# Performance work log

Hardware: AMD Instinct MI355X
Metric: run time of the kernel (lower is better)

## Reference

```python
import jax, jax.numpy as jnp
import numpy as np

N = 50000        # num nodes (num_paths)
E = 1_600_000    # num edges (avg degree 32)
W = 64           # window_size -> x feature dim
H = 128          # hidden_dimension
TEMP = 1.0       # temperature


def setup_inputs() -> dict:
    key = jax.random.key(0)
    k = jax.random.split(key, 6)
    x = jax.random.normal(k[0], (N, W), dtype=jnp.float32)
    y = jax.random.normal(k[1], (N,), dtype=jnp.float32)
    edge_index = jax.random.randint(k[2], (2, E), 0, N, dtype=jnp.int32)
    w1 = jax.random.normal(k[3], (2 * W, H), dtype=jnp.float32) / np.sqrt(2 * W)
    b1 = jnp.zeros((H,), dtype=jnp.float32)
    w2 = jax.random.normal(k[4], (H, 1), dtype=jnp.float32) / np.sqrt(H)
    b2 = jnp.zeros((1,), dtype=jnp.float32)
    return {"x": x, "y": y, "edge_index": edge_index,
            "w1": w1, "b1": b1, "w2": w2, "b2": b2}


def reference(x, y, edge_index, w1, b1, w2, b2):
    src, dst = edge_index[0], edge_index[1]
    # edge-wise gather + concat: [E, 2W]
    feat = jnp.concatenate([x[src], x[dst]], axis=1)
    # attention MLP: Linear -> ReLU -> Linear
    h = jax.nn.relu(feat @ w1 + b1)          # [E, H]
    logits = (h @ w2 + b2)[:, 0] / TEMP      # [E]
    # segment softmax over destination nodes (numerically stable)
    m = jax.ops.segment_max(logits, dst, num_segments=N)      # [N]
    e = jnp.exp(logits - m[dst])                               # [E]
    denom = jax.ops.segment_sum(e, dst, num_segments=N)       # [N]
    alpha = e / denom[dst]                                     # [E]
    # weighted scatter-sum aggregation
    y_hat = jax.ops.segment_sum(y[src] * alpha, dst, num_segments=N)  # [N]
    return y_hat, alpha[:, None]
```

## Files before the change

kernel.cpp:

```cpp
#include <hip/hip_runtime.h>
#include <hip/hip_bf16.h>

#define QSCALE 44.0f

__device__ __forceinline__ unsigned short f2bf(float f) {
    unsigned u = __float_as_uint(f);
    unsigned r = (u + 0x7fffu + ((u >> 16) & 1u)) >> 16;
    return (unsigned short)r;
}
__device__ __forceinline__ float bfu(unsigned short s) {
    return __uint_as_float(((unsigned)s) << 16);
}

__device__ __forceinline__ float dot4_i8(unsigned ax, unsigned bx, const float* w) {
    float acc = 0.f;
#pragma unroll
    for (int i = 0; i < 4; ++i) {
        int va = (int)(char)(ax >> (8 * i));
        int vb = (int)(char)(bx >> (8 * i));
        acc += w[i] * (float)max(va + vb, 0);
    }
    return acc;
}

__device__ __forceinline__ float edge_dot(const uint4& a, const uint4& b, const float* w2r) {
    float acc;
    acc  = dot4_i8(a.x, b.x, w2r + 0);
    acc += dot4_i8(a.y, b.y, w2r + 4);
    acc += dot4_i8(a.z, b.z, w2r + 8);
    acc += dot4_i8(a.w, b.w, w2r + 12);
    acc += __shfl_xor(acc, 1);
    acc += __shfl_xor(acc, 2);
    acc += __shfl_xor(acc, 4);
    return acc;
}

__device__ __forceinline__ unsigned long long pack_contrib(float ev, float ys) {
    float flo = fminf(ev * 65536.f, 1.0e9f);
    float fhi = fmaxf(fminf(ys * ev * 16384.f, 1.0e9f), -1.0e9f);
    unsigned int qlo = (unsigned int)__float2int_rn(flo);
    int          qhi = __float2int_rn(fhi);
    return ((unsigned long long)(unsigned int)qhi << 32) | (unsigned long long)qlo;
}

__global__ __launch_bounds__(256) void proj_kernel(
    const float* __restrict__ x, const float* __restrict__ w1, const float* __restrict__ b1,
    unsigned char* __restrict__ P, unsigned long long* __restrict__ agg, int N)
{
    __shared__ unsigned short wl[64 * 256];
    __shared__ float xs[32 * 64];
    const int t = threadIdx.x;

    for (int i = t; i < 64 * 256; i += 256) {
        int k = i >> 8, j = i & 255;
        float w = (j < 128) ? w1[k * 128 + j] : w1[(64 + k) * 128 + (j - 128)];
        wl[i] = f2bf(w);
    }

    const int jg = t & 63;
    const int ng = t >> 6;
    const int j0 = jg * 4;

    float bb[4] = {0.f, 0.f, 0.f, 0.f};
    if (j0 < 128) {
#pragma unroll
        for (int c = 0; c < 4; ++c) bb[c] = b1[j0 + c];
    }

    const int ntiles = (N + 31) / 32;
    for (int tile = blockIdx.x; tile < ntiles; tile += gridDim.x) {
        const int n0 = tile * 32;

        __syncthreads();
        if (t < 32) {
            int n = n0 + t;
            if (n < N) agg[n] = 0ull;
        }
        for (int i = t; i < 32 * 64; i += 256) {
            int n = n0 + (i >> 6);
            xs[i] = (n < N) ? x[(size_t)n * 64 + (i & 63)] : 0.f;
        }
        __syncthreads();

        float acc[8][4];
#pragma unroll
        for (int i = 0; i < 8; ++i)
#pragma unroll
            for (int c = 0; c < 4; ++c) acc[i][c] = 0.f;

        for (int k = 0; k < 64; k += 4) {
            float wv[4][4];
#pragma unroll
            for (int kk = 0; kk < 4; ++kk) {
                ushort4 wu = *(const ushort4*)&wl[(k + kk) * 256 + j0];
                wv[kk][0] = bfu(wu.x); wv[kk][1] = bfu(wu.y);
                wv[kk][2] = bfu(wu.z); wv[kk][3] = bfu(wu.w);
            }
#pragma unroll
            for (int i = 0; i < 8; ++i) {
                const float4 xv = *(const float4*)&xs[(ng * 8 + i) * 64 + k];
#pragma unroll
                for (int c = 0; c < 4; ++c)
                    acc[i][c] += xv.x * wv[0][c] + xv.y * wv[1][c] + xv.z * wv[2][c] + xv.w * wv[3][c];
            }
        }

#pragma unroll
        for (int i = 0; i < 8; ++i) {
            int n = n0 + ng * 8 + i;
            if (n < N) {
                unsigned pk = 0;
#pragma unroll
                for (int c = 0; c < 4; ++c) {
                    float v = (acc[i][c] + bb[c]) * QSCALE;
                    int q = __float2int_rn(fminf(fmaxf(v, -127.f), 127.f));
                    pk |= ((unsigned)(q & 0xff)) << (8 * c);
                }
                *(unsigned*)(P + (size_t)n * 256 + j0) = pk;
            }
        }
    }
}

__global__ __launch_bounds__(256) void edge_logit_kernel(
    const unsigned char* __restrict__ P, const int* __restrict__ ei,
    const float* __restrict__ y,
    const float* __restrict__ w2, const float* __restrict__ b2,
    float* __restrict__ elog, unsigned long long* __restrict__ agg, int E)
{
    const int lane = threadIdx.x & 7;
    float w2r[16];
#pragma unroll
    for (int c = 0; c < 16; ++c) w2r[c] = w2[lane * 16 + c] * (1.0f / QSCALE);
    const float b2s = b2[0];

    const int slot = (blockIdx.x * 256 + threadIdx.x) >> 3;
    const int nslots = (gridDim.x * 256) >> 3;
    const int lo16 = lane * 16;

    for (int base = slot * 4; base < E; base += nslots * 4) {
        if (base + 3 < E) {
            const int4 s4 = *(const int4*)&ei[base];
            const int4 d4 = *(const int4*)&ei[E + base];

            const uint4 a0 = *(const uint4*)(P + (size_t)s4.x * 256 + lo16);
            const uint4 b0 = *(const uint4*)(P + (size_t)d4.x * 256 + 128 + lo16);
            const uint4 a1 = *(const uint4*)(P + (size_t)s4.y * 256 + lo16);
            const uint4 b1 = *(const uint4*)(P + (size_t)d4.y * 256 + 128 + lo16);
            const uint4 a2 = *(const uint4*)(P + (size_t)s4.z * 256 + lo16);
            const uint4 b2v = *(const uint4*)(P + (size_t)d4.z * 256 + 128 + lo16);
            const uint4 a3 = *(const uint4*)(P + (size_t)s4.w * 256 + lo16);
            const uint4 b3 = *(const uint4*)(P + (size_t)d4.w * 256 + 128 + lo16);

            const float acc0 = edge_dot(a0, b0, w2r);
            const float acc1 = edge_dot(a1, b1, w2r);
            const float acc2 = edge_dot(a2, b2v, w2r);
            const float acc3 = edge_dot(a3, b3, w2r);

            if (lane == 0) {
                const float ys0 = y[s4.x];
                const float ys1 = y[s4.y];
                const float ys2 = y[s4.z];
                const float ys3 = y[s4.w];
                const float ev0 = __expf(acc0 + b2s);
                const float ev1 = __expf(acc1 + b2s);
                const float ev2 = __expf(acc2 + b2s);
                const float ev3 = __expf(acc3 + b2s);
                *(float4*)&elog[base] = make_float4(ev0, ev1, ev2, ev3);
                atomicAdd(&agg[d4.x], pack_contrib(ev0, ys0));
                atomicAdd(&agg[d4.y], pack_contrib(ev1, ys1));
                atomicAdd(&agg[d4.z], pack_contrib(ev2, ys2));
                atomicAdd(&agg[d4.w], pack_contrib(ev3, ys3));
            }
        } else {
            for (int e = base; e < E; ++e) {
                const int s = ei[e];
                const int d = ei[E + e];
                const uint4 a = *(const uint4*)(P + (size_t)s * 256 + lo16);
                const uint4 b = *(const uint4*)(P + (size_t)d * 256 + 128 + lo16);
                const float acc = edge_dot(a, b, w2r);
                if (lane == 0) {
                    const float ev = __expf(acc + b2s);
                    elog[e] = ev;
                    atomicAdd(&agg[d], pack_contrib(ev, y[s]));
                }
            }
        }
    }
}

__global__ void node_decode_kernel(const unsigned long long* __restrict__ agg,
                                   float* __restrict__ inv_d,
                                   float* __restrict__ yhat, int N) {
    int i = blockIdx.x * 256 + threadIdx.x;
    if (i >= N) return;
    unsigned long long v = agg[i];
    unsigned int lo = (unsigned int)(v & 0xffffffffull);
    int          hi = (int)(v >> 32);
    if (lo != 0u) {
        float flo = (float)lo;
        yhat[i]  = 4.0f * (float)hi / flo;
        inv_d[i] = 65536.0f / flo;
    } else {
        yhat[i]  = 0.f;
        inv_d[i] = 0.f;
    }
}

__global__ __launch_bounds__(256) void alpha_norm_kernel(
    const int* __restrict__ ei, float* __restrict__ elog,
    const float* __restrict__ inv_d, int E)
{
    const int base = (blockIdx.x * 256 + threadIdx.x) * 4;
    if (base + 3 < E) {
        const int4   d4  = *(const int4*)&ei[E + base];
        float4       ev4 = *(const float4*)&elog[base];
        ev4.x *= inv_d[d4.x];
        ev4.y *= inv_d[d4.y];
        ev4.z *= inv_d[d4.z];
        ev4.w *= inv_d[d4.w];
        *(float4*)&elog[base] = ev4;
    } else {
        for (int e = base; e < E; ++e)
            elog[e] = elog[e] * inv_d[ei[E + e]];
    }
}

extern "C" void kernel_launch(void* const* d_in, const int* in_sizes, int n_in,
                              void* d_out, int out_size, void* d_ws, size_t ws_size,
                              hipStream_t stream) {
    const float* x  = (const float*)d_in[0];
    const float* y  = (const float*)d_in[1];
    const int*   ei = (const int*)d_in[2];
    const float* w1 = (const float*)d_in[3];
    const float* b1 = (const float*)d_in[4];
    const float* w2 = (const float*)d_in[5];
    const float* b2 = (const float*)d_in[6];

    const int N = in_sizes[1];
    const int E = in_sizes[2] / 2;

    float* out  = (float*)d_out;
    float* yhat = out;
    float* elog = out + N;

    char* ws = (char*)d_ws;
    unsigned char* P = (unsigned char*)ws;
    size_t Pbytes = (size_t)N * 256;
    unsigned long long* agg = (unsigned long long*)(ws + Pbytes);
    float* inv_d = (float*)(ws + Pbytes + (size_t)N * 8);

    proj_kernel<<<512, 256, 0, stream>>>(x, w1, b1, P, agg, N);
    edge_logit_kernel<<<2048, 256, 0, stream>>>(P, ei, y, w2, b2, elog, agg, E);
    node_decode_kernel<<<(N + 255) / 256, 256, 0, stream>>>(agg, inv_d, yhat, N);
    alpha_norm_kernel<<<(E / 4 + 255) / 256, 256, 0, stream>>>(ei, elog, inv_d, E);
}
```

Measured before the change: 212.4 us.

## Fuse four kernels into one persistent kernel with software grid barriers

```diff
diff --git a/kernel.cpp b/kernel.cpp
--- a/kernel.cpp
+++ b/kernel.cpp
@@ -1,7 +1,9 @@
 #include <hip/hip_runtime.h>
-#include <hip/hip_bf16.h>
 
 #define QSCALE 44.0f
+#define NBLK 768
+#define NTHR 256
+#define NT (NBLK * NTHR)
 
 __device__ __forceinline__ unsigned short f2bf(float f) {
     unsigned u = __float_as_uint(f);
@@ -43,186 +45,200 @@
     return ((unsigned long long)(unsigned int)qhi << 32) | (unsigned long long)qlo;
 }
 
-__global__ __launch_bounds__(256) void proj_kernel(
-    const float* __restrict__ x, const float* __restrict__ w1, const float* __restrict__ b1,
-    unsigned char* __restrict__ P, unsigned long long* __restrict__ agg, int N)
+__device__ __forceinline__ void grid_sync(unsigned long long* bar) {
+    __syncthreads();
+    if (threadIdx.x == 0) {
+        __threadfence();
+        unsigned long long t = atomicAdd(bar, 1ull) + 1ull;
+        unsigned long long target = ((t + (unsigned long long)NBLK - 1ull)
+                                     / (unsigned long long)NBLK) * (unsigned long long)NBLK;
+        while (__hip_atomic_load(bar, __ATOMIC_RELAXED, __HIP_MEMORY_SCOPE_AGENT) < target)
+            __builtin_amdgcn_s_sleep(2);
+        __threadfence();
+    }
+    __syncthreads();
+}
+
+__global__ __launch_bounds__(NTHR) void fused_gat_kernel(
+    const float* __restrict__ x, const float* __restrict__ y,
+    const int* __restrict__ ei,
+    const float* __restrict__ w1, const float* __restrict__ b1,
+    const float* __restrict__ w2, const float* __restrict__ b2,
+    unsigned char* __restrict__ P, unsigned long long* __restrict__ agg,
+    unsigned long long* __restrict__ bar,
+    float* __restrict__ yhat, float* __restrict__ elog, int N, int E)
 {
     __shared__ unsigned short wl[64 * 256];
     __shared__ float xs[32 * 64];
     const int t = threadIdx.x;
-
-    for (int i = t; i < 64 * 256; i += 256) {
-        int k = i >> 8, j = i & 255;
-        float w = (j < 128) ? w1[k * 128 + j] : w1[(64 + k) * 128 + (j - 128)];
-        wl[i] = f2bf(w);
-    }
-
-    const int jg = t & 63;
-    const int ng = t >> 6;
-    const int j0 = jg * 4;
-
-    float bb[4] = {0.f, 0.f, 0.f, 0.f};
-    if (j0 < 128) {
-#pragma unroll
-        for (int c = 0; c < 4; ++c) bb[c] = b1[j0 + c];
-    }
-
-    const int ntiles = (N + 31) / 32;
-    for (int tile = blockIdx.x; tile < ntiles; tile += gridDim.x) {
-        const int n0 = tile * 32;
-
-        __syncthreads();
-        if (t < 32) {
-            int n = n0 + t;
-            if (n < N) agg[n] = 0ull;
-        }
-        for (int i = t; i < 32 * 64; i += 256) {
-            int n = n0 + (i >> 6);
-            xs[i] = (n < N) ? x[(size_t)n * 64 + (i & 63)] : 0.f;
-        }
-        __syncthreads();
-
-        float acc[8][4];
-#pragma unroll
-        for (int i = 0; i < 8; ++i)
-#pragma unroll
-            for (int c = 0; c < 4; ++c) acc[i][c] = 0.f;
-
-        for (int k = 0; k < 64; k += 4) {
-            float wv[4][4];
-#pragma unroll
-            for (int kk = 0; kk < 4; ++kk) {
-                ushort4 wu = *(const ushort4*)&wl[(k + kk) * 256 + j0];
-                wv[kk][0] = bfu(wu.x); wv[kk][1] = bfu(wu.y);
-                wv[kk][2] = bfu(wu.z); wv[kk][3] = bfu(wu.w);
-            }
+    const int gtid = blockIdx.x * NTHR + t;
+
+    {
+        for (int i = t; i < 64 * 256; i += NTHR) {
+            int k = i >> 8, j = i & 255;
+            float w = (j < 128) ? w1[k * 128 + j] : w1[(64 + k) * 128 + (j - 128)];
+            wl[i] = f2bf(w);
+        }
+
+        const int jg = t & 63;
+        const int ng = t >> 6;
+        const int j0 = jg * 4;
+
+        float bb[4] = {0.f, 0.f, 0.f, 0.f};
+        if (j0 < 128) {
+#pragma unroll
+            for (int c = 0; c < 4; ++c) bb[c] = b1[j0 + c];
+        }
+
+        const int ntiles = (N + 31) / 32;
+        for (int tile = blockIdx.x; tile < ntiles; tile += NBLK) {
+            const int n0 = tile * 32;
+
+            __syncthreads();
+            if (t < 32) {
+                int n = n0 + t;
+                if (n < N) agg[n] = 0ull;
+            }
+            for (int i = t; i < 32 * 64; i += NTHR) {
+                int n = n0 + (i >> 6);
+                xs[i] = (n < N) ? x[(size_t)n * 64 + (i & 63)] : 0.f;
+            }
+            __syncthreads();
+
+            float acc[8][4];
+#pragma unroll
+            for (int i = 0; i < 8; ++i)
+#pragma unroll
+                for (int c = 0; c < 4; ++c) acc[i][c] = 0.f;
+
+            for (int k = 0; k < 64; k += 4) {
+                float wv[4][4];
+#pragma unroll
+                for (int kk = 0; kk < 4; ++kk) {
+                    ushort4 wu = *(const ushort4*)&wl[(k + kk) * 256 + j0];
+                    wv[kk][0] = bfu(wu.x); wv[kk][1] = bfu(wu.y);
+                    wv[kk][2] = bfu(wu.z); wv[kk][3] = bfu(wu.w);
+                }
+#pragma unroll
+                for (int i = 0; i < 8; ++i) {
+                    const float4 xv = *(const float4*)&xs[(ng * 8 + i) * 64 + k];
+#pragma unroll
+                    for (int c = 0; c < 4; ++c)
+                        acc[i][c] += xv.x * wv[0][c] + xv.y * wv[1][c] + xv.z * wv[2][c] + xv.w * wv[3][c];
+                }
+            }
+
 #pragma unroll
             for (int i = 0; i < 8; ++i) {
-                const float4 xv = *(const float4*)&xs[(ng * 8 + i) * 64 + k];
-#pragma unroll
-                for (int c = 0; c < 4; ++c)
-                    acc[i][c] += xv.x * wv[0][c] + xv.y * wv[1][c] + xv.z * wv[2][c] + xv.w * wv[3][c];
-            }
-        }
-
-#pragma unroll
-        for (int i = 0; i < 8; ++i) {
-            int n = n0 + ng * 8 + i;
-            if (n < N) {
-                unsigned pk = 0;
-#pragma unroll
-                for (int c = 0; c < 4; ++c) {
-                    float v = (acc[i][c] + bb[c]) * QSCALE;
-                    int q = __float2int_rn(fminf(fmaxf(v, -127.f), 127.f));
-                    pk |= ((unsigned)(q & 0xff)) << (8 * c);
-                }
-                *(unsigned*)(P + (size_t)n * 256 + j0) = pk;
-            }
-        }
-    }
-}
-
-__global__ __launch_bounds__(256) void edge_logit_kernel(
-    const unsigned char* __restrict__ P, const int* __restrict__ ei,
-    const float* __restrict__ y,
-    const float* __restrict__ w2, const float* __restrict__ b2,
-    float* __restrict__ elog, unsigned long long* __restrict__ agg, int E)
-{
-    const int lane = threadIdx.x & 7;
-    float w2r[16];
-#pragma unroll
-    for (int c = 0; c < 16; ++c) w2r[c] = w2[lane * 16 + c] * (1.0f / QSCALE);
-    const float b2s = b2[0];
-
-    const int slot = (blockIdx.x * 256 + threadIdx.x) >> 3;
-    const int nslots = (gridDim.x * 256) >> 3;
-    const int lo16 = lane * 16;
-
-    for (int base = slot * 4; base < E; base += nslots * 4) {
-        if (base + 3 < E) {
-            const int4 s4 = *(const int4*)&ei[base];
-            const int4 d4 = *(const int4*)&ei[E + base];
-
-            const uint4 a0 = *(const uint4*)(P + (size_t)s4.x * 256 + lo16);
-            const uint4 b0 = *(const uint4*)(P + (size_t)d4.x * 256 + 128 + lo16);
-            const uint4 a1 = *(const uint4*)(P + (size_t)s4.y * 256 + lo16);
-            const uint4 b1 = *(const uint4*)(P + (size_t)d4.y * 256 + 128 + lo16);
-            const uint4 a2 = *(const uint4*)(P + (size_t)s4.z * 256 + lo16);
-            const uint4 b2v = *(const uint4*)(P + (size_t)d4.z * 256 + 128 + lo16);
-            const uint4 a3 = *(const uint4*)(P + (size_t)s4.w * 256 + lo16);
-            const uint4 b3 = *(const uint4*)(P + (size_t)d4.w * 256 + 128 + lo16);
-
-            const float acc0 = edge_dot(a0, b0, w2r);
-            const float acc1 = edge_dot(a1, b1, w2r);
-            const float acc2 = edge_dot(a2, b2v, w2r);
-            const float acc3 = edge_dot(a3, b3, w2r);
-
-            if (lane == 0) {
-                const float ys0 = y[s4.x];
-                const float ys1 = y[s4.y];
-                const float ys2 = y[s4.z];
-                const float ys3 = y[s4.w];
-                const float ev0 = __expf(acc0 + b2s);
-                const float ev1 = __expf(acc1 + b2s);
-                const float ev2 = __expf(acc2 + b2s);
-                const float ev3 = __expf(acc3 + b2s);
-                *(float4*)&elog[base] = make_float4(ev0, ev1, ev2, ev3);
-                atomicAdd(&agg[d4.x], pack_contrib(ev0, ys0));
-                atomicAdd(&agg[d4.y], pack_contrib(ev1, ys1));
-                atomicAdd(&agg[d4.z], pack_contrib(ev2, ys2));
-                atomicAdd(&agg[d4.w], pack_contrib(ev3, ys3));
-            }
-        } else {
-            for (int e = base; e < E; ++e) {
-                const int s = ei[e];
-                const int d = ei[E + e];
-                const uint4 a = *(const uint4*)(P + (size_t)s * 256 + lo16);
-                const uint4 b = *(const uint4*)(P + (size_t)d * 256 + 128 + lo16);
-                const float acc = edge_dot(a, b, w2r);
+                int n = n0 + ng * 8 + i;
+                if (n < N) {
+                    unsigned pk = 0;
+#pragma unroll
+                    for (int c = 0; c < 4; ++c) {
+                        float v = (acc[i][c] + bb[c]) * QSCALE;
+                        int q = __float2int_rn(fminf(fmaxf(v, -127.f), 127.f));
+                        pk |= ((unsigned)(q & 0xff)) << (8 * c);
+                    }
+                    *(unsigned*)(P + (size_t)n * 256 + j0) = pk;
+                }
+            }
+        }
+    }
+
+    grid_sync(bar);
+
+    {
+        const int lane = t & 7;
+        float w2r[16];
+#pragma unroll
+        for (int c = 0; c < 16; ++c) w2r[c] = w2[lane * 16 + c] * (1.0f / QSCALE);
+        const float b2s = b2[0];
+
+        const int slot = gtid >> 3;
+        const int nslots = NT >> 3;
+        const int lo16 = lane * 16;
+
+        for (int base = slot * 4; base < E; base += nslots * 4) {
+            if (base + 3 < E) {
+                const int4 s4 = *(const int4*)&ei[base];
+                const int4 d4 = *(const int4*)&ei[E + base];
+
+                const uint4 a0 = *(const uint4*)(P + (size_t)s4.x * 256 + lo16);
+                const uint4 b0 = *(const uint4*)(P + (size_t)d4.x * 256 + 128 + lo16);
+                const uint4 a1 = *(const uint4*)(P + (size_t)s4.y * 256 + lo16);
+                const uint4 b1v = *(const uint4*)(P + (size_t)d4.y * 256 + 128 + lo16);
+                const uint4 a2 = *(const uint4*)(P + (size_t)s4.z * 256 + lo16);
+                const uint4 b2v = *(const uint4*)(P + (size_t)d4.z * 256 + 128 + lo16);
+                const uint4 a3 = *(const uint4*)(P + (size_t)s4.w * 256 + lo16);
+                const uint4 b3 = *(const uint4*)(P + (size_t)d4.w * 256 + 128 + lo16);
+
+                const float acc0 = edge_dot(a0, b0, w2r);
+                const float acc1 = edge_dot(a1, b1v, w2r);
+                const float acc2 = edge_dot(a2, b2v, w2r);
+                const float acc3 = edge_dot(a3, b3, w2r);
+
                 if (lane == 0) {
-                    const float ev = __expf(acc + b2s);
-                    elog[e] = ev;
-                    atomicAdd(&agg[d], pack_contrib(ev, y[s]));
-                }
-            }
-        }
-    }
-}
-
-__global__ void node_decode_kernel(const unsigned long long* __restrict__ agg,
-                                   float* __restrict__ inv_d,
-                                   float* __restrict__ yhat, int N) {
-    int i = blockIdx.x * 256 + threadIdx.x;
-    if (i >= N) return;
-    unsigned long long v = agg[i];
-    unsigned int lo = (unsigned int)(v & 0xffffffffull);
-    int          hi = (int)(v >> 32);
-    if (lo != 0u) {
-        float flo = (float)lo;
-        yhat[i]  = 4.0f * (float)hi / flo;
-        inv_d[i] = 65536.0f / flo;
-    } else {
-        yhat[i]  = 0.f;
-        inv_d[i] = 0.f;
-    }
-}
-
-__global__ __launch_bounds__(256) void alpha_norm_kernel(
-    const int* __restrict__ ei, float* __restrict__ elog,
-    const float* __restrict__ inv_d, int E)
-{
-    const int base = (blockIdx.x * 256 + threadIdx.x) * 4;
-    if (base + 3 < E) {
-        const int4   d4  = *(const int4*)&ei[E + base];
-        float4       ev4 = *(const float4*)&elog[base];
-        ev4.x *= inv_d[d4.x];
-        ev4.y *= inv_d[d4.y];
-        ev4.z *= inv_d[d4.z];
-        ev4.w *= inv_d[d4.w];
-        *(float4*)&elog[base] = ev4;
-    } else {
-        for (int e = base; e < E; ++e)
-            elog[e] = elog[e] * inv_d[ei[E + e]];
+                    const float ys0 = y[s4.x];
+                    const float ys1 = y[s4.y];
+                    const float ys2 = y[s4.z];
+                    const float ys3 = y[s4.w];
+                    const float ev0 = __expf(acc0 + b2s);
+                    const float ev1 = __expf(acc1 + b2s);
+                    const float ev2 = __expf(acc2 + b2s);
+                    const float ev3 = __expf(acc3 + b2s);
+                    *(float4*)&elog[base] = make_float4(ev0, ev1, ev2, ev3);
+                    atomicAdd(&agg[d4.x], pack_contrib(ev0, ys0));
+                    atomicAdd(&agg[d4.y], pack_contrib(ev1, ys1));
+                    atomicAdd(&agg[d4.z], pack_contrib(ev2, ys2));
+                    atomicAdd(&agg[d4.w], pack_contrib(ev3, ys3));
+                }
+            } else {
+                for (int e = base; e < E; ++e) {
+                    const int s = ei[e];
+                    const int d = ei[E + e];
+                    const uint4 a = *(const uint4*)(P + (size_t)s * 256 + lo16);
+                    const uint4 b = *(const uint4*)(P + (size_t)d * 256 + 128 + lo16);
+                    const float acc = edge_dot(a, b, w2r);
+                    if (lane == 0) {
+                        const float ev = __expf(acc + b2s);
+                        elog[e] = ev;
+                        atomicAdd(&agg[d], pack_contrib(ev, y[s]));
+                    }
+                }
+            }
+        }
+    }
+
+    grid_sync(bar);
+
+    {
+        for (int i = gtid; i < N; i += NT) {
+            unsigned long long v = agg[i];
+            unsigned int lo = (unsigned int)(v & 0xffffffffull);
+            int          hi = (int)(v >> 32);
+            yhat[i] = (lo != 0u) ? 4.0f * (float)hi / (float)lo : 0.f;
+        }
+
+        for (int base = gtid * 4; base < E; base += NT * 4) {
+            if (base + 3 < E) {
+                const int4 d4 = *(const int4*)&ei[E + base];
+                float4 ev4 = *(const float4*)&elog[base];
+                const unsigned int l0 = (unsigned int)(agg[d4.x] & 0xffffffffull);
+                const unsigned int l1 = (unsigned int)(agg[d4.y] & 0xffffffffull);
+                const unsigned int l2 = (unsigned int)(agg[d4.z] & 0xffffffffull);
+                const unsigned int l3 = (unsigned int)(agg[d4.w] & 0xffffffffull);
+                ev4.x = l0 ? ev4.x * (65536.0f / (float)l0) : 0.f;
+                ev4.y = l1 ? ev4.y * (65536.0f / (float)l1) : 0.f;
+                ev4.z = l2 ? ev4.z * (65536.0f / (float)l2) : 0.f;
+                ev4.w = l3 ? ev4.w * (65536.0f / (float)l3) : 0.f;
+                *(float4*)&elog[base] = ev4;
+            } else {
+                for (int e = base; e < E; ++e) {
+                    const unsigned int lo = (unsigned int)(agg[ei[E + e]] & 0xffffffffull);
+                    elog[e] = lo ? elog[e] * (65536.0f / (float)lo) : 0.f;
+                }
+            }
+        }
     }
 }
 
@@ -245,13 +261,12 @@
     float* elog = out + N;
 
     char* ws = (char*)d_ws;
-    unsigned char* P = (unsigned char*)ws;
-    size_t Pbytes = (size_t)N * 256;
-    unsigned long long* agg = (unsigned long long*)(ws + Pbytes);
-    float* inv_d = (float*)(ws + Pbytes + (size_t)N * 8);
-
-    proj_kernel<<<512, 256, 0, stream>>>(x, w1, b1, P, agg, N);
-    edge_logit_kernel<<<2048, 256, 0, stream>>>(P, ei, y, w2, b2, elog, agg, E);
-    node_decode_kernel<<<(N + 255) / 256, 256, 0, stream>>>(agg, inv_d, yhat, N);
-    alpha_norm_kernel<<<(E / 4 + 255) / 256, 256, 0, stream>>>(ei, elog, inv_d, E);
-}
+    unsigned long long* bar = (unsigned long long*)ws;
+    unsigned char* P = (unsigned char*)(ws + 256);
+    const size_t Pbytes = (size_t)N * 256;
+    unsigned long long* agg = (unsigned long long*)(ws + 256 + Pbytes);
+
+    hipMemsetAsync(bar, 0, 8, stream);
+    fused_gat_kernel<<<NBLK, NTHR, 0, stream>>>(
+        x, y, ei, w1, b1, w2, b2, P, agg, bar, yhat, elog, N, E);
+}
```

Measured after the change: 372.5 us. 75.4% more time.
